# Optimization experiments

Hardware: AMD Instinct MI355X
Metric: run time of the kernel (lower is better)

The kernel has to match this reference:

```python
import jax, jax.numpy as jnp
import numpy as np

B, S, D, H = 2, 2048, 2048, 16
HD = D // H            # 128
HALF = HD // 2         # 64
SOFTCAP = 50.0
ROPE_BASE = 10000.0


def setup_inputs() -> dict:
    key = jax.random.key(0)
    k1, k2, k3 = jax.random.split(key, 3)
    inputs = jax.random.normal(k1, (B, S, D), dtype=jnp.float32)
    # param init ~ nnx.initializers.normal() (stddev 0.01 default; scale to keep activations sane)
    w_in = jax.random.normal(k2, (D, H, 3 * HD), dtype=jnp.float32) * (1.0 / np.sqrt(D))
    w_out = jax.random.normal(k3, (H, HD, D), dtype=jnp.float32) * (1.0 / np.sqrt(D))
    # RoPE tables: [S, HALF]
    pos = jnp.arange(S, dtype=jnp.float32)[:, None]
    inv_freq = 1.0 / (ROPE_BASE ** (jnp.arange(HALF, dtype=jnp.float32) / HALF))
    ang = pos * inv_freq[None, :]
    rope_sin = jnp.sin(ang)
    rope_cos = jnp.cos(ang)
    # causal mask [1, 1, S, S]
    mask = jnp.tril(jnp.ones((S, S), dtype=bool))[None, None, :, :]
    return {"inputs": inputs, "w_in": w_in, "w_out": w_out,
            "rope_sin": rope_sin, "rope_cos": rope_cos, "mask": mask}


def apply_rope(x, sin, cos):
    # x: [B, S, H, HD]; sin/cos: [S, HALF] -> broadcast [1, S, 1, HALF]
    sin = sin[None, :, None, :]
    cos = cos[None, :, None, :]
    x1, x2 = x[..., :HALF], x[..., HALF:]
    return jnp.concatenate([x1 * cos - x2 * sin, x2 * cos + x1 * sin], axis=-1)


def reference(inputs, w_in, w_out, rope_sin, rope_cos, mask):
    dtype = inputs.dtype
    # fused QKV projection: [B, S, H, 3*HD]
    qkv = jnp.einsum('bsd,bhf->bshf'.replace('bhf', 'dhf'), inputs, w_in)
    q, k, v = jnp.split(qkv, 3, axis=-1)           # each [B, S, H, HD]
    q = apply_rope(q, rope_sin, rope_cos)
    k = apply_rope(k, rope_sin, rope_cos)
    q = q / jnp.sqrt(jnp.asarray(HD, dtype))
    scores = jnp.einsum('bqhd,bkhd->bhqk', q, k)   # [B, H, S, S]
    big_neg = jnp.finfo(dtype).min
    scores = jnp.where(mask, scores, big_neg)
    scores = jnp.tanh(scores / SOFTCAP) * SOFTCAP  # softcap
    attn = jax.nn.softmax(scores, axis=-1)
    x = jnp.einsum('bhqk,bkhd->bqhd', attn, v)     # [B, S, H, HD]
    out = jnp.einsum('bqhd,hdm->bqm', x, w_out)    # [B, S, D]
    return out
```

## Files before the change

### kernel.cpp

```cpp
#include <hip/hip_runtime.h>

#define B_ 2
#define S_ 2048
#define D_ 2048
#define H_ 16
#define HD_ 128
#define NT_ (S_ / 64)
#define NBUF 6

typedef unsigned short u16;
typedef __bf16 bf16x8 __attribute__((ext_vector_type(8)));
typedef float f32x4 __attribute__((ext_vector_type(4)));

__device__ __forceinline__ float bf2f(u16 u) {
  unsigned int x = ((unsigned int)u) << 16;
  return __builtin_bit_cast(float, x);
}
__device__ __forceinline__ u16 f2bf(float f) {
  unsigned int u = __builtin_bit_cast(unsigned int, f);
  u += 0x7fffu + ((u >> 16) & 1u);
  return (u16)(u >> 16);
}
__device__ __forceinline__ void async16(const void* g, void* l) {
  __builtin_amdgcn_global_load_lds((const __attribute__((address_space(1))) void*)g,
                                   (__attribute__((address_space(3))) void*)l, 16, 0, 0);
}
__device__ __forceinline__ float vexp2(float x) {
  float r;
  asm("v_exp_f32 %0, %1" : "=v"(r) : "v"(x));
  return r;
}
__device__ __forceinline__ float vrcp(float x) {
  float r;
  asm("v_rcp_f32 %0, %1" : "=v"(r) : "v"(x));
  return r;
}

__global__ __launch_bounds__(256) void conv_f32_bf16(const float* __restrict__ in,
                                                     u16* __restrict__ outp, int n) {
  int idx = (blockIdx.x * 256 + threadIdx.x) * 4;
  int stride = gridDim.x * 256 * 4;
  for (; idx < n; idx += stride) {
    float4 v = *(const float4*)(in + idx);
    ushort4 ov = make_ushort4(f2bf(v.x), f2bf(v.y), f2bf(v.z), f2bf(v.w));
    *(ushort4*)(outp + idx) = ov;
  }
}

__global__ __launch_bounds__(256) void transpose_conv(const float* __restrict__ in,
                                                      u16* __restrict__ outp, int R, int C) {
  __shared__ float tile[32][33];
  int c0 = blockIdx.x * 32, r0 = blockIdx.y * 32;
  int tx = threadIdx.x & 31, ty = threadIdx.x >> 5;
#pragma unroll
  for (int yy = 0; yy < 32; yy += 8)
    tile[ty + yy][tx] = in[(size_t)(r0 + ty + yy) * C + c0 + tx];
  __syncthreads();
#pragma unroll
  for (int yy = 0; yy < 32; yy += 8)
    outp[(size_t)(c0 + ty + yy) * R + r0 + tx] = f2bf(tile[tx][ty + yy]);
}

__global__ __launch_bounds__(256) void transpose_win(const float* __restrict__ in,
                                                     u16* __restrict__ outp) {
  __shared__ float tile[32][33];
  int n0 = blockIdx.x * 32, k0 = blockIdx.y * 32;
  int tx = threadIdx.x & 31, ty = threadIdx.x >> 5;
  int n = n0 + tx;
  int cc = n >> 7, p = n & 127;
  int q = (p >> 4) & 3;
  int d = ((p >> 6) << 5) + ((q >> 1) << 4) + ((q & 1) << 6) + (p & 15);
  int f = (cc / 3) * 384 + (cc % 3) * 128 + d;
#pragma unroll
  for (int yy = 0; yy < 32; yy += 8)
    tile[ty + yy][tx] = in[(size_t)(k0 + ty + yy) * 6144 + f];
  __syncthreads();
#pragma unroll
  for (int yy = 0; yy < 32; yy += 8)
    outp[(size_t)(n0 + ty + yy) * 2048 + k0 + tx] = f2bf(tile[tx][ty + yy]);
}

#define BAR __builtin_amdgcn_s_barrier()
#define LGKM0                                          \
  {                                                    \
    asm volatile("s_waitcnt lgkmcnt(0)" ::: "memory"); \
    __builtin_amdgcn_sched_barrier(0);                 \
  }
#define VM4 asm volatile("s_waitcnt vmcnt(4)" ::: "memory")
#define VM0 asm volatile("s_waitcnt vmcnt(0)" ::: "memory")
#define P1 __builtin_amdgcn_s_setprio(1)
#define P0 __builtin_amdgcn_s_setprio(0)

template <int EPI>
__global__ __launch_bounds__(512, 1) void gemm256_8p(
    const u16* __restrict__ A, const u16* __restrict__ Bt, float* __restrict__ C, int K, int N,
    int ntn, u16* __restrict__ Qo, u16* __restrict__ Ko, u16* __restrict__ Vo,
    const float* __restrict__ rsin, const float* __restrict__ rcos) {
  __shared__ alignas(16) u16 lsA[2][256 * 64];
  __shared__ alignas(16) u16 lsB[2][256 * 64];
  const int tid = threadIdx.x;
  const int lane = tid & 63, wid = tid >> 6;
  const int g = lane >> 4, lr = lane & 15;
  const int wm = wid >> 2, wn = wid & 3;

  const int nwg = 16 * ntn;
  const int bid = blockIdx.x;
  const int swz = (bid & 7) * (nwg >> 3) + (bid >> 3);
  const int m_idx = swz & 15, n_idx = swz >> 4;
  const size_t m0 = (size_t)m_idx * 256, n0 = (size_t)n_idx * 256;

  const int row0 = tid >> 3, sl0 = tid & 7;
  const int row1 = (512 + tid) >> 3, sl1 = tid & 7;
  const u16* pA0 = A + (m0 + row0) * K + ((sl0 ^ (row0 & 7)) << 3);
  const u16* pA1 = A + (m0 + row1) * K + ((sl1 ^ (row1 & 7)) << 3);
  const u16* pB0 = Bt + (n0 + row0) * K + ((sl0 ^ (row0 & 7)) << 3);
  const u16* pB1 = Bt + (n0 + row1) * K + ((sl1 ^ (row1 & 7)) << 3);
  const size_t hstep = (size_t)128 * K;

#define STG_A(t, buf, half)                                                                        \
  {                                                                                                \
    async16(pA0 + (half)*hstep + (size_t)(t)*64, (char*)lsA[buf] + (half)*16384 + tid * 16);       \
    async16(pA1 + (half)*hstep + (size_t)(t)*64, (char*)lsA[buf] + (half)*16384 + 8192 + tid * 16); \
  }
#define STG_B(t, buf, half)                                                                        \
  {                                                                                                \
    async16(pB0 + (half)*hstep + (size_t)(t)*64, (char*)lsB[buf] + (half)*16384 + tid * 16);       \
    async16(pB1 + (half)*hstep + (size_t)(t)*64, (char*)lsB[buf] + (half)*16384 + 8192 + tid * 16); \
  }

  const int sw0 = ((g) ^ (lr & 7)) << 4;
  const int sw1 = ((4 + g) ^ (lr & 7)) << 4;

#define LDA(tb, mh)                                                                      \
  {                                                                                      \
    _Pragma("unroll") for (int i2 = 0; i2 < 4; ++i2) {                                   \
      const char* _p = (const char*)lsA[tb] + (wm * 128 + (mh)*64 + i2 * 16 + lr) * 128; \
      aF[i2][0] = *(const bf16x8*)(_p + sw0);                                            \
      aF[i2][1] = *(const bf16x8*)(_p + sw1);                                            \
    }                                                                                    \
  }
#define LDB(tb, dst, nh)                                                                \
  {                                                                                     \
    _Pragma("unroll") for (int j2 = 0; j2 < 2; ++j2) {                                  \
      const char* _p = (const char*)lsB[tb] + (wn * 64 + (nh)*32 + j2 * 16 + lr) * 128; \
      dst[j2][0] = *(const bf16x8*)(_p + sw0);                                          \
      dst[j2][1] = *(const bf16x8*)(_p + sw1);                                          \
    }                                                                                   \
  }
#define MM(mh, nh, BB)                                                                       \
  {                                                                                          \
    _Pragma("unroll") for (int i2 = 0; i2 < 4; ++i2) _Pragma("unroll") for (int j2 = 0;     \
                                                                            j2 < 2; ++j2) { \
      acc[(mh)*4 + i2][(nh)*2 + j2] = __builtin_amdgcn_mfma_f32_16x16x32_bf16(               \
          aF[i2][0], BB[j2][0], acc[(mh)*4 + i2][(nh)*2 + j2], 0, 0, 0);                     \
      acc[(mh)*4 + i2][(nh)*2 + j2] = __builtin_amdgcn_mfma_f32_16x16x32_bf16(               \
          aF[i2][1], BB[j2][1], acc[(mh)*4 + i2][(nh)*2 + j2], 0, 0, 0);                     \
    }                                                                                        \
  }

  f32x4 acc[8][4] = {};
  const int nk2 = K >> 7;

  STG_A(0, 0, 0);
  STG_B(0, 0, 1);
  STG_B(0, 0, 0);
  STG_A(0, 0, 1);
  STG_A(1, 1, 0);
  STG_B(1, 1, 1);
  VM4;
  BAR;

  bf16x8 aF[4][2], b0[2][2], b1[2][2];
#pragma unroll 1
  for (int it = 0; it < nk2 - 1; ++it) {
    const int t1 = 2 * it + 1, s2 = 2 * it + 2, s3 = 2 * it + 3;
    LDA(0, 0);
    LDB(0, b0, 0);
    STG_B(t1, 1, 0);
    BAR; LGKM0; P1; MM(0, 0, b0); P0; BAR;
    LDB(0, b1, 1);
    STG_A(t1, 1, 1);
    BAR; LGKM0; P1; MM(0, 1, b1); P0; BAR;
    LDA(0, 1);
    STG_A(s2, 0, 0);
    BAR; LGKM0; P1; MM(1, 1, b1); P0; BAR;
    STG_B(s2, 0, 1);
    BAR; LGKM0; P1; MM(1, 0, b0); P0;
    VM4;
    BAR;
    LDA(1, 0);
    LDB(1, b0, 0);
    STG_B(s2, 0, 0);
    BAR; LGKM0; P1; MM(0, 0, b0); P0; BAR;
    LDB(1, b1, 1);
    STG_A(s2, 0, 1);
    BAR; LGKM0; P1; MM(0, 1, b1); P0; BAR;
    LDA(1, 1);
    STG_A(s3, 1, 0);
    BAR; LGKM0; P1; MM(1, 1, b1); P0; BAR;
    STG_B(s3, 1, 1);
    BAR; LGKM0; P1; MM(1, 0, b0); P0;
    VM4;
    BAR;
  }
  {
    const int t1 = 2 * (nk2 - 1) + 1;
    LDA(0, 0);
    LDB(0, b0, 0);
    STG_B(t1, 1, 0);
    BAR; LGKM0; P1; MM(0, 0, b0); P0; BAR;
    LDB(0, b1, 1);
    STG_A(t1, 1, 1);
    BAR; LGKM0; P1; MM(0, 1, b1); P0; BAR;
    LDA(0, 1);
    BAR; LGKM0; P1; MM(1, 1, b1); P0; BAR;
    BAR; LGKM0; P1; MM(1, 0, b0); P0;
    VM0;
    BAR;
    LDA(1, 0);
    LDB(1, b0, 0);
    BAR; LGKM0; P1; MM(0, 0, b0); P0; BAR;
    LDB(1, b1, 1);
    BAR; LGKM0; P1; MM(0, 1, b1); P0; BAR;
    LDA(1, 1);
    BAR; LGKM0; P1; MM(1, 1, b1); P0; BAR;
    BAR; LGKM0; P1; MM(1, 0, b0); P0; BAR;
  }
#undef STG_A
#undef STG_B
#undef LDA
#undef LDB
#undef MM

  if (EPI == 0) {
#pragma unroll
    for (int ai = 0; ai < 8; ++ai)
#pragma unroll
      for (int bj = 0; bj < 4; ++bj)
#pragma unroll
        for (int r = 0; r < 4; ++r) {
          size_t m = m0 + wm * 128 + (ai >> 2) * 64 + (ai & 3) * 16 + 4 * g + r;
          size_t n = n0 + wn * 64 + (bj >> 1) * 32 + (bj & 1) * 16 + lr;
          C[m * N + n] = acc[ai][bj][r];
        }
  } else {
    const int c = (int)(n0 >> 7) + (wn >> 1);
    const int h = c / 3, part = c % 3;
    const int wn1 = wn & 1;
    if (part == 2) {
#pragma unroll
      for (int ai = 0; ai < 8; ++ai) {
        int m = (int)m0 + wm * 128 + (ai >> 2) * 64 + (ai & 3) * 16 + 4 * g;
        int b = m >> 11, s = m & (S_ - 1);
#pragma unroll
        for (int bj = 0; bj < 4; ++bj) {
          int hd = wn1 * 32 + ((bj >> 1) << 4) + ((bj & 1) << 6) + lr;
          ushort4 pk;
          pk.x = f2bf(acc[ai][bj][0]);
          pk.y = f2bf(acc[ai][bj][1]);
          pk.z = f2bf(acc[ai][bj][2]);
          pk.w = f2bf(acc[ai][bj][3]);
          *(ushort4*)(Vo + ((size_t)(b * H_ + h) * HD_ + hd) * S_ + s) = pk;
        }
      }
    } else {
      u16* dstp = (part == 0) ? Qo : Ko;
      const float scl = (part == 0) ? 0.08838834764831845f : 1.0f;
#pragma unroll
      for (int ai = 0; ai < 8; ++ai) {
        int mbase = (int)m0 + wm * 128 + (ai >> 2) * 64 + (ai & 3) * 16 + 4 * g;
#pragma unroll
        for (int r = 0; r < 4; ++r) {
          int m = mbase + r;
          int b = m >> 11, s = m & (S_ - 1);
          const float* srow = rsin + s * 64;
          const float* crow = rcos + s * 64;
          u16* op = dstp + ((size_t)(b * H_ + h) * S_ + s) * HD_;
#pragma unroll
          for (int t = 0; t < 2; ++t) {
            int d = wn1 * 32 + t * 16 + lr;
            float cv = crow[d] * scl, sv = srow[d] * scl;
            float x1 = acc[ai][t * 2][r], x2 = acc[ai][t * 2 + 1][r];
            op[d] = f2bf(x1 * cv - x2 * sv);
            op[d + 64] = f2bf(x2 * cv + x1 * sv);
          }
        }
      }
    }
  }
}

template <int EPI>
__global__ __launch_bounds__(512, 1) void gemm8p(const u16* __restrict__ A,
                                                 const u16* __restrict__ Bt,
                                                 float* __restrict__ C, int K, int N, int gx,
                                                 u16* __restrict__ Qo, u16* __restrict__ Ko,
                                                 u16* __restrict__ Vo) {
  __shared__ alignas(16) u16 lsA[NBUF][256 * 32];
  __shared__ alignas(16) u16 lsB[NBUF][128 * 32];
  const int tid = threadIdx.x;
  const int lane = tid & 63;
  const int wid = tid >> 6;
  const int g = lane >> 4, lr = lane & 15;
  const int wm = wid >> 1, wn = wid & 1;

  const int nwg = gx << 4;
  const int bid = blockIdx.x;
  const int swz = (bid & 7) * (nwg >> 3) + (bid >> 3);
  const int m_idx = swz & 15, n_idx = swz >> 4;
  const size_t m0 = (size_t)m_idx * 256, n0 = (size_t)n_idx * 128;

  const int la0 = tid, la1 = 512 + tid;
  const int rowA0 = la0 >> 2, slA0 = la0 & 3;
  const int rowA1 = la1 >> 2, slA1 = la1 & 3;
  const int rowB = tid >> 2, slB = tid & 3;
  const u16* srcA0 = A + (m0 + rowA0) * K + ((slA0 ^ ((rowA0 >> 1) & 3)) << 3);
  const u16* srcA1 = A + (m0 + rowA1) * K + ((slA1 ^ ((rowA1 >> 1) & 3)) << 3);
  const u16* srcB = Bt + (n0 + rowB) * K + ((slB ^ ((rowB >> 1) & 3)) << 3);

#define STAGE(t, bufi)                                  \
  {                                                     \
    const int koff = (t) << 5;                          \
    async16(srcA0 + koff, (char*)lsA[bufi] + la0 * 16); \
    async16(srcA1 + koff, (char*)lsA[bufi] + la1 * 16); \
    async16(srcB + koff, (char*)lsB[bufi] + tid * 16);  \
  }

  int ofsA[4], ofsB[4];
#pragma unroll
  for (int i = 0; i < 4; ++i) {
    int ra = wm * 64 + i * 16 + lr;
    ofsA[i] = ra * 64 + ((g ^ ((ra >> 1) & 3)) << 4);
    int rb = wn * 64 + i * 16 + lr;
    ofsB[i] = rb * 64 + ((g ^ ((rb >> 1) & 3)) << 4);
  }

  f32x4 acc[4][4] = {};
  const int nk = K >> 5;

#pragma unroll
  for (int t = 0; t < NBUF - 1; ++t) STAGE(t, t);
  asm volatile("s_waitcnt vmcnt(12)" ::: "memory");
  __builtin_amdgcn_s_barrier();

  int buf = 0;
#pragma unroll 1
  for (int kt = 0; kt < nk; ++kt) {
    bf16x8 af[4], bfr[4];
#pragma unroll
    for (int i = 0; i < 4; ++i) af[i] = *(const bf16x8*)((const char*)lsA[buf] + ofsA[i]);
#pragma unroll
    for (int j = 0; j < 4; ++j) bfr[j] = *(const bf16x8*)((const char*)lsB[buf] + ofsB[j]);
    const int st = kt + NBUF - 1;
    const int sbuf = buf == 0 ? NBUF - 1 : buf - 1;
    if (st < nk) STAGE(st, sbuf);
    __builtin_amdgcn_s_barrier();
    __builtin_amdgcn_s_setprio(1);
#pragma unroll
    for (int i = 0; i < 4; ++i)
#pragma unroll
      for (int j = 0; j < 4; ++j)
        acc[i][j] = __builtin_amdgcn_mfma_f32_16x16x32_bf16(af[i], bfr[j], acc[i][j], 0, 0, 0);
    __builtin_amdgcn_s_setprio(0);
    asm volatile("s_waitcnt vmcnt(12)" ::: "memory");
    __builtin_amdgcn_s_barrier();
    buf = buf == NBUF - 1 ? 0 : buf + 1;
  }
#undef STAGE

  if (EPI == 0) {
#pragma unroll
    for (int i = 0; i < 4; ++i)
#pragma unroll
      for (int j = 0; j < 4; ++j)
#pragma unroll
        for (int r = 0; r < 4; ++r) {
          size_t m = m0 + wm * 64 + i * 16 + 4 * g + r;
          size_t n = n0 + wn * 64 + j * 16 + lr;
          C[m * N + n] = acc[i][j][r];
        }
  } else {
    const int part = n_idx % 3, h = n_idx / 3;
    u16* dst = (part == 0) ? Qo : (part == 1 ? Ko : Vo);
#pragma unroll
    for (int i = 0; i < 4; ++i)
#pragma unroll
      for (int j = 0; j < 4; ++j)
#pragma unroll
        for (int r = 0; r < 4; ++r) {
          int m = (int)m0 + wm * 64 + i * 16 + 4 * g + r;
          int hd = wn * 64 + j * 16 + lr;
          int b = m >> 11, s = m & (S_ - 1);
          dst[((size_t)(b * H_ + h) * S_ + s) * HD_ + hd] = f2bf(acc[i][j][r]);
        }
  }
}

__global__ __launch_bounds__(256) void attn_fwd(const u16* __restrict__ Q, const u16* __restrict__ K,
                                                const u16* __restrict__ VT, u16* __restrict__ X) {
  const int bx = blockIdx.x;
  const int bh = blockIdx.y;
  const int tid = threadIdx.x;
  const int lane = tid & 63, wid = tid >> 6;
  const int g = lane >> 4, lr = lane & 15;

  __shared__ alignas(16) u16 lsK[2][64 * 128];
  __shared__ alignas(16) u16 lsV[2][128 * 64];
  __shared__ alignas(16) u16 lsP[4][16 * 72];

  const u16* Qp = Q + (size_t)bh * S_ * HD_;
  const u16* Kp = K + (size_t)bh * S_ * HD_;
  const u16* Vp = VT + (size_t)bh * HD_ * S_;
  u16* myP = lsP[wid];
  const int b = bh >> 4, h = bh & 15;

  const float c1 = -0.057707802f;
  const float c2 = -144.26950409f;

#pragma unroll 1
  for (int pass = 0; pass < 2; ++pass) {
    const int qt = pass ? bx : (NT_ - 1 - bx);
    const int qrow = qt * 64 + wid * 16 + lr;
    const int qbase = qt * 64 + wid * 16 + 4 * g;

    bf16x8 qf[4];
#pragma unroll
    for (int kc = 0; kc < 4; ++kc)
      qf[kc] = *(const bf16x8*)(Qp + (size_t)qrow * HD_ + kc * 32 + g * 8);

    f32x4 o[8] = {};
    float psum[4] = {0.f, 0.f, 0.f, 0.f};

#pragma unroll
    for (int p = 0; p < 4; ++p) {
      int c = p * 256 + tid;
      int rowk = c >> 4;
      int wsk = ((c & 15) << 4) ^ ((rowk & 7) << 4);
      async16((const char*)Kp + (((size_t)rowk) << 8) + wsk, (char*)lsK[0] + c * 16);
      int rowv = c >> 3;
      int wsv = ((c & 7) << 4) ^ ((rowv & 7) << 4);
      async16((const char*)Vp + (size_t)rowv * (S_ * 2) + wsv, (char*)lsV[0] + c * 16);
    }
    __syncthreads();

    int cur = 0;
    for (int kt = 0; kt <= qt; ++kt) {
      if (kt < qt) {
        const int nxt = kt + 1;
#pragma unroll
        for (int p = 0; p < 4; ++p) {
          int c = p * 256 + tid;
          int rowk = c >> 4;
          int wsk = ((c & 15) << 4) ^ ((rowk & 7) << 4);
          async16((const char*)Kp + (((size_t)(nxt * 64 + rowk)) << 8) + wsk,
                  (char*)lsK[cur ^ 1] + c * 16);
          int rowv = c >> 3;
          int wsv = ((c & 7) << 4) ^ ((rowv & 7) << 4);
          async16((const char*)Vp + (size_t)rowv * (S_ * 2) + nxt * 128 + wsv,
                  (char*)lsV[cur ^ 1] + c * 16);
        }
      }
      f32x4 sc[4];
#pragma unroll
      for (int jn = 0; jn < 4; ++jn) {
        f32x4 a = {0.f, 0.f, 0.f, 0.f};
        const int row = jn * 16 + lr;
        const int sw = (row & 7) << 4;
#pragma unroll
        for (int kc = 0; kc < 4; ++kc) {
          int w = (kc * 64 + g * 16) ^ sw;
          bf16x8 kf = *(const bf16x8*)((const char*)lsK[cur] + row * 256 + w);
          a = __builtin_amdgcn_mfma_f32_16x16x32_bf16(qf[kc], kf, a, 0, 0, 0);
        }
        sc[jn] = a;
      }
#pragma unroll
      for (int jn = 0; jn < 4; ++jn) {
        int key = kt * 64 + jn * 16 + lr;
#pragma unroll
        for (int r = 0; r < 4; ++r) {
          float z = vexp2(c1 * sc[jn][r]);
          float p = vexp2(c2 * z * vrcp(1.f + z));
          if (key > qbase + r) p = 0.f;
          psum[r] += p;
          myP[(4 * g + r) * 72 + jn * 16 + lr] = f2bf(p);
        }
      }
#pragma unroll
      for (int kc = 0; kc < 2; ++kc) {
        bf16x8 pa = *(const bf16x8*)(myP + lr * 72 + kc * 32 + g * 8);
#pragma unroll
        for (int jh = 0; jh < 8; ++jh) {
          int row = jh * 16 + lr;
          int w = (kc * 64 + g * 16) ^ ((row & 7) << 4);
          bf16x8 vf = *(const bf16x8*)((const char*)lsV[cur] + row * 128 + w);
          o[jh] = __builtin_amdgcn_mfma_f32_16x16x32_bf16(pa, vf, o[jh], 0, 0, 0);
        }
      }
      __syncthreads();
      cur ^= 1;
    }
    float lsum[4];
#pragma unroll
    for (int r = 0; r < 4; ++r) {
      float s = psum[r];
#pragma unroll
      for (int msk = 1; msk < 16; msk <<= 1) s += __shfl_xor(s, msk, 64);
      lsum[r] = s;
    }
#pragma unroll
    for (int r = 0; r < 4; ++r) {
      float inv = 1.f / lsum[r];
      int s = qbase + r;
      u16* xp = X + ((size_t)(b * S_ + s)) * D_ + h * HD_;
#pragma unroll
      for (int jh = 0; jh < 8; ++jh) xp[jh * 16 + lr] = f2bf(o[jh][r] * inv);
    }
  }
}

extern "C" void kernel_launch(void* const* d_in, const int* in_sizes, int n_in,
                              void* d_out, int out_size, void* d_ws, size_t ws_size,
                              hipStream_t stream) {
  const float* inputs = (const float*)d_in[0];
  const float* w_in = (const float*)d_in[1];
  const float* w_out = (const float*)d_in[2];
  const float* rsin = (const float*)d_in[3];
  const float* rcos = (const float*)d_in[4];
  float* out = (float*)d_out;

  char* ws = (char*)d_ws;
  u16* bfA = (u16*)(ws);
  u16* w_inT = (u16*)(ws + 16777216);
  u16* Qraw = (u16*)(ws + 41943040);
  u16* Kraw = (u16*)(ws + 58720256);
  u16* VT = (u16*)(ws + 75497472);
  u16* Xbuf = (u16*)(ws);
  u16* w_outT = (u16*)(ws + 16777216);

  conv_f32_bf16<<<2048, 256, 0, stream>>>(inputs, bfA, B_ * S_ * D_);
  transpose_win<<<dim3(192, 64), 256, 0, stream>>>(w_in, w_inT);
  gemm256_8p<1><<<384, 512, 0, stream>>>(bfA, w_inT, nullptr, 2048, 6144, 24, Qraw, Kraw, VT,
                                         rsin, rcos);
  transpose_conv<<<dim3(64, 64), 256, 0, stream>>>(w_out, w_outT, 2048, 2048);
  attn_fwd<<<dim3(NT_ / 2, 32), 256, 0, stream>>>(Qraw, Kraw, VT, Xbuf);
  gemm8p<0><<<256, 512, 0, stream>>>(Xbuf, w_outT, out, 2048, 2048, 16,
                                     nullptr, nullptr, nullptr);
}
```

Measured before the change: 288.3 us.

## Use 8-wave attention blocks sharing K/V tiles and vectorize Q/K/X stores via permuted layouts

The attention kernel now runs 512 threads per block, with two groups of four waves each handling one of two adjacent 64-row query tiles. Both groups share each K/V LDS tile, and the lower group skips the final key tile, so K/V staging traffic per query row is halved. The RoPE epilogue and the attention output now write packed ushort4 and 8-wide vectors instead of scalar bf16 stores. To keep results correct, the head dimension is permuted: w_out is transposed with a matching row permutation so the output GEMM sees the correct ordering. Grid size drops to 256 blocks and the lower group idles for one tile each pass, which may hurt load balance.

```diff
diff --git a/kernel.cpp b/kernel.cpp
--- a/kernel.cpp
+++ b/kernel.cpp
@@ -11,6 +11,7 @@
 typedef unsigned short u16;
 typedef __bf16 bf16x8 __attribute__((ext_vector_type(8)));
 typedef float f32x4 __attribute__((ext_vector_type(4)));
+typedef u16 u16x8 __attribute__((ext_vector_type(8)));
 
 __device__ __forceinline__ float bf2f(u16 u) {
   unsigned int x = ((unsigned int)u) << 16;
@@ -45,20 +46,6 @@
     ushort4 ov = make_ushort4(f2bf(v.x), f2bf(v.y), f2bf(v.z), f2bf(v.w));
     *(ushort4*)(outp + idx) = ov;
   }
-}
-
-__global__ __launch_bounds__(256) void transpose_conv(const float* __restrict__ in,
-                                                      u16* __restrict__ outp, int R, int C) {
-  __shared__ float tile[32][33];
-  int c0 = blockIdx.x * 32, r0 = blockIdx.y * 32;
-  int tx = threadIdx.x & 31, ty = threadIdx.x >> 5;
-#pragma unroll
-  for (int yy = 0; yy < 32; yy += 8)
-    tile[ty + yy][tx] = in[(size_t)(r0 + ty + yy) * C + c0 + tx];
-  __syncthreads();
-#pragma unroll
-  for (int yy = 0; yy < 32; yy += 8)
-    outp[(size_t)(c0 + ty + yy) * R + r0 + tx] = f2bf(tile[tx][ty + yy]);
 }
 
 __global__ __launch_bounds__(256) void transpose_win(const float* __restrict__ in,
@@ -74,6 +61,24 @@
 #pragma unroll
   for (int yy = 0; yy < 32; yy += 8)
     tile[ty + yy][tx] = in[(size_t)(k0 + ty + yy) * 6144 + f];
+  __syncthreads();
+#pragma unroll
+  for (int yy = 0; yy < 32; yy += 8)
+    outp[(size_t)(n0 + ty + yy) * 2048 + k0 + tx] = f2bf(tile[tx][ty + yy]);
+}
+
+__global__ __launch_bounds__(256) void transpose_wout(const float* __restrict__ in,
+                                                      u16* __restrict__ outp) {
+  __shared__ float tile[32][33];
+  int k0 = blockIdx.x * 32, n0 = blockIdx.y * 32;
+  int tx = threadIdx.x & 31, ty = threadIdx.x >> 5;
+#pragma unroll
+  for (int yy = 0; yy < 32; yy += 8) {
+    int kk = k0 + ty + yy;
+    int hh = kk >> 7, j = kk & 127;
+    int hd = (j & 7) * 16 + (j >> 3);
+    tile[ty + yy][tx] = in[(size_t)(hh * 128 + hd) * 2048 + n0 + tx];
+  }
   __syncthreads();
 #pragma unroll
   for (int yy = 0; yy < 32; yy += 8)
@@ -275,15 +280,22 @@
           int b = m >> 11, s = m & (S_ - 1);
           const float* srow = rsin + s * 64;
           const float* crow = rcos + s * 64;
-          u16* op = dstp + ((size_t)(b * H_ + h) * S_ + s) * HD_;
+          u16* op = dstp + ((size_t)(b * H_ + h) * S_ + s) * HD_ + ((wn1 * 16 + lr) << 2);
+          ushort4 pk;
 #pragma unroll
           for (int t = 0; t < 2; ++t) {
             int d = wn1 * 32 + t * 16 + lr;
             float cv = crow[d] * scl, sv = srow[d] * scl;
             float x1 = acc[ai][t * 2][r], x2 = acc[ai][t * 2 + 1][r];
-            op[d] = f2bf(x1 * cv - x2 * sv);
-            op[d + 64] = f2bf(x2 * cv + x1 * sv);
+            if (t == 0) {
+              pk.x = f2bf(x1 * cv - x2 * sv);
+              pk.y = f2bf(x2 * cv + x1 * sv);
+            } else {
+              pk.z = f2bf(x1 * cv - x2 * sv);
+              pk.w = f2bf(x2 * cv + x1 * sv);
+            }
           }
+          *(ushort4*)op = pk;
         }
       }
     }
@@ -379,34 +391,22 @@
           size_t n = n0 + wn * 64 + j * 16 + lr;
           C[m * N + n] = acc[i][j][r];
         }
-  } else {
-    const int part = n_idx % 3, h = n_idx / 3;
-    u16* dst = (part == 0) ? Qo : (part == 1 ? Ko : Vo);
-#pragma unroll
-    for (int i = 0; i < 4; ++i)
-#pragma unroll
-      for (int j = 0; j < 4; ++j)
-#pragma unroll
-        for (int r = 0; r < 4; ++r) {
-          int m = (int)m0 + wm * 64 + i * 16 + 4 * g + r;
-          int hd = wn * 64 + j * 16 + lr;
-          int b = m >> 11, s = m & (S_ - 1);
-          dst[((size_t)(b * H_ + h) * S_ + s) * HD_ + hd] = f2bf(acc[i][j][r]);
-        }
-  }
-}
-
-__global__ __launch_bounds__(256) void attn_fwd(const u16* __restrict__ Q, const u16* __restrict__ K,
-                                                const u16* __restrict__ VT, u16* __restrict__ X) {
+  }
+}
+
+__global__ __launch_bounds__(512, 1) void attn_fwd(const u16* __restrict__ Q, const u16* __restrict__ K,
+                                                   const u16* __restrict__ VT, u16* __restrict__ X) {
   const int bx = blockIdx.x;
   const int bh = blockIdx.y;
   const int tid = threadIdx.x;
   const int lane = tid & 63, wid = tid >> 6;
   const int g = lane >> 4, lr = lane & 15;
+  const int wq = wid & 3;
+  const int tb = wid >> 2;
 
   __shared__ alignas(16) u16 lsK[2][64 * 128];
   __shared__ alignas(16) u16 lsV[2][128 * 64];
-  __shared__ alignas(16) u16 lsP[4][16 * 72];
+  __shared__ alignas(16) u16 lsP[8][16 * 72];
 
   const u16* Qp = Q + (size_t)bh * S_ * HD_;
   const u16* Kp = K + (size_t)bh * S_ * HD_;
@@ -419,9 +419,11 @@
 
 #pragma unroll 1
   for (int pass = 0; pass < 2; ++pass) {
-    const int qt = pass ? bx : (NT_ - 1 - bx);
-    const int qrow = qt * 64 + wid * 16 + lr;
-    const int qbase = qt * 64 + wid * 16 + 4 * g;
+    const int u = pass ? bx : (15 - bx);
+    const int qa = 2 * u, qb = qa + 1;
+    const int qt = qa + tb;
+    const int qrow = qt * 64 + wq * 16 + lr;
+    const int qbase = qt * 64 + wq * 16 + 4 * g;
 
     bf16x8 qf[4];
 #pragma unroll
@@ -432,8 +434,8 @@
     float psum[4] = {0.f, 0.f, 0.f, 0.f};
 
 #pragma unroll
-    for (int p = 0; p < 4; ++p) {
-      int c = p * 256 + tid;
+    for (int p = 0; p < 2; ++p) {
+      int c = p * 512 + tid;
       int rowk = c >> 4;
       int wsk = ((c & 15) << 4) ^ ((rowk & 7) << 4);
       async16((const char*)Kp + (((size_t)rowk) << 8) + wsk, (char*)lsK[0] + c * 16);
@@ -444,12 +446,12 @@
     __syncthreads();
 
     int cur = 0;
-    for (int kt = 0; kt <= qt; ++kt) {
-      if (kt < qt) {
+    for (int kt = 0; kt <= qb; ++kt) {
+      if (kt < qb) {
         const int nxt = kt + 1;
 #pragma unroll
-        for (int p = 0; p < 4; ++p) {
-          int c = p * 256 + tid;
+        for (int p = 0; p < 2; ++p) {
+          int c = p * 512 + tid;
           int rowk = c >> 4;
           int wsk = ((c & 15) << 4) ^ ((rowk & 7) << 4);
           async16((const char*)Kp + (((size_t)(nxt * 64 + rowk)) << 8) + wsk,
@@ -460,41 +462,43 @@
                   (char*)lsV[cur ^ 1] + c * 16);
         }
       }
-      f32x4 sc[4];
-#pragma unroll
-      for (int jn = 0; jn < 4; ++jn) {
-        f32x4 a = {0.f, 0.f, 0.f, 0.f};
-        const int row = jn * 16 + lr;
-        const int sw = (row & 7) << 4;
-#pragma unroll
-        for (int kc = 0; kc < 4; ++kc) {
-          int w = (kc * 64 + g * 16) ^ sw;
-          bf16x8 kf = *(const bf16x8*)((const char*)lsK[cur] + row * 256 + w);
-          a = __builtin_amdgcn_mfma_f32_16x16x32_bf16(qf[kc], kf, a, 0, 0, 0);
-        }
-        sc[jn] = a;
-      }
-#pragma unroll
-      for (int jn = 0; jn < 4; ++jn) {
-        int key = kt * 64 + jn * 16 + lr;
-#pragma unroll
-        for (int r = 0; r < 4; ++r) {
-          float z = vexp2(c1 * sc[jn][r]);
-          float p = vexp2(c2 * z * vrcp(1.f + z));
-          if (key > qbase + r) p = 0.f;
-          psum[r] += p;
-          myP[(4 * g + r) * 72 + jn * 16 + lr] = f2bf(p);
-        }
-      }
-#pragma unroll
-      for (int kc = 0; kc < 2; ++kc) {
-        bf16x8 pa = *(const bf16x8*)(myP + lr * 72 + kc * 32 + g * 8);
-#pragma unroll
-        for (int jh = 0; jh < 8; ++jh) {
-          int row = jh * 16 + lr;
-          int w = (kc * 64 + g * 16) ^ ((row & 7) << 4);
-          bf16x8 vf = *(const bf16x8*)((const char*)lsV[cur] + row * 128 + w);
-          o[jh] = __builtin_amdgcn_mfma_f32_16x16x32_bf16(pa, vf, o[jh], 0, 0, 0);
+      if (tb | (kt <= qa)) {
+        f32x4 sc[4];
+#pragma unroll
+        for (int jn = 0; jn < 4; ++jn) {
+          f32x4 a = {0.f, 0.f, 0.f, 0.f};
+          const int row = jn * 16 + lr;
+          const int sw = (row & 7) << 4;
+#pragma unroll
+          for (int kc = 0; kc < 4; ++kc) {
+            int w = (kc * 64 + g * 16) ^ sw;
+            bf16x8 kf = *(const bf16x8*)((const char*)lsK[cur] + row * 256 + w);
+            a = __builtin_amdgcn_mfma_f32_16x16x32_bf16(qf[kc], kf, a, 0, 0, 0);
+          }
+          sc[jn] = a;
+        }
+#pragma unroll
+        for (int jn = 0; jn < 4; ++jn) {
+          int key = kt * 64 + jn * 16 + lr;
+#pragma unroll
+          for (int r = 0; r < 4; ++r) {
+            float z = vexp2(c1 * sc[jn][r]);
+            float p = vexp2(c2 * z * vrcp(1.f + z));
+            if (key > qbase + r) p = 0.f;
+            psum[r] += p;
+            myP[(4 * g + r) * 72 + jn * 16 + lr] = f2bf(p);
+          }
+        }
+#pragma unroll
+        for (int kc = 0; kc < 2; ++kc) {
+          bf16x8 pa = *(const bf16x8*)(myP + lr * 72 + kc * 32 + g * 8);
+#pragma unroll
+          for (int jh = 0; jh < 8; ++jh) {
+            int row = jh * 16 + lr;
+            int w = (kc * 64 + g * 16) ^ ((row & 7) << 4);
+            bf16x8 vf = *(const bf16x8*)((const char*)lsV[cur] + row * 128 + w);
+            o[jh] = __builtin_amdgcn_mfma_f32_16x16x32_bf16(pa, vf, o[jh], 0, 0, 0);
+          }
         }
       }
       __syncthreads();
@@ -512,9 +516,10 @@
     for (int r = 0; r < 4; ++r) {
       float inv = 1.f / lsum[r];
       int s = qbase + r;
-      u16* xp = X + ((size_t)(b * S_ + s)) * D_ + h * HD_;
-#pragma unroll
-      for (int jh = 0; jh < 8; ++jh) xp[jh * 16 + lr] = f2bf(o[jh][r] * inv);
+      u16x8 pk;
+#pragma unroll
+      for (int jh = 0; jh < 8; ++jh) pk[jh] = f2bf(o[jh][r] * inv);
+      *(u16x8*)(X + ((size_t)(b * S_ + s)) * D_ + h * HD_ + lr * 8) = pk;
     }
   }
 }
@@ -542,8 +547,8 @@
   transpose_win<<<dim3(192, 64), 256, 0, stream>>>(w_in, w_inT);
   gemm256_8p<1><<<384, 512, 0, stream>>>(bfA, w_inT, nullptr, 2048, 6144, 24, Qraw, Kraw, VT,
                                          rsin, rcos);
-  transpose_conv<<<dim3(64, 64), 256, 0, stream>>>(w_out, w_outT, 2048, 2048);
-  attn_fwd<<<dim3(NT_ / 2, 32), 256, 0, stream>>>(Qraw, Kraw, VT, Xbuf);
+  transpose_wout<<<dim3(64, 64), 256, 0, stream>>>(w_out, w_outT);
+  attn_fwd<<<dim3(8, 32), 512, 0, stream>>>(Qraw, Kraw, VT, Xbuf);
   gemm8p<0><<<256, 512, 0, stream>>>(Xbuf, w_outT, out, 2048, 2048, 16,
                                      nullptr, nullptr, nullptr);
 }
```

New measurement: 289.8 us. No clear change (+0.5%).
